# Performance work log

Measured on AMD Instinct MI355X. Metric: run time of the kernel, lower is better.

## Reference

```python
import jax, jax.numpy as jnp
import numpy as np

NEG_SLOPE = 0.2  # PyG GATConv default leaky_relu slope

def _glorot(key, shape):
    fan_in, fan_out = shape[0], shape[1]
    lim = jnp.sqrt(6.0 / (fan_in + fan_out))
    return jax.random.uniform(key, shape, jnp.float32, -lim, lim)

def setup_inputs() -> dict:
    key = jax.random.key(0)
    ks = jax.random.split(key, 16)
    N, E, S = 20000, 640000, 32
    in_dim, hid, out = 384, 128, 64
    inp = {
        'persona_x': jax.random.normal(ks[0], (N, in_dim), jnp.float32),
        'persona_edge_index': jax.random.randint(ks[1], (2, E), 0, N, jnp.int64),
        'story_x': jax.random.normal(ks[2], (S, N, in_dim), jnp.float32),
        'story_edge_index': jax.random.randint(ks[3], (S, 2, E), 0, N, jnp.int64),
    }
    # persona GAT params
    inp['p_W1'] = _glorot(ks[4], (in_dim, hid)); inp['p_a1'] = _glorot(ks[5], (2 * hid, 1)).reshape(2 * hid)
    inp['p_b1'] = jnp.zeros((hid,), jnp.float32)
    inp['p_W2'] = _glorot(ks[6], (hid, out)); inp['p_a2'] = _glorot(ks[7], (2 * out, 1)).reshape(2 * out)
    inp['p_b2'] = jnp.zeros((out,), jnp.float32)
    # story GAT params
    inp['s_W1'] = _glorot(ks[8], (in_dim, hid)); inp['s_a1'] = _glorot(ks[9], (2 * hid, 1)).reshape(2 * hid)
    inp['s_b1'] = jnp.zeros((hid,), jnp.float32)
    inp['s_W2'] = _glorot(ks[10], (hid, out)); inp['s_a2'] = _glorot(ks[11], (2 * out, 1)).reshape(2 * out)
    inp['s_b2'] = jnp.zeros((out,), jnp.float32)
    inp['temperature'] = jnp.asarray(0.07, jnp.float32)
    return inp

def gat_conv(x, edge_index, W, a, b):
    # x: [N, F_in], edge_index: [2, E] (row 0 = src, row 1 = dst), PyG GATConv heads=1
    N = x.shape[0]
    h = x @ W  # [N, F_out]
    src, dst = edge_index[0], edge_index[1]
    F_out = h.shape[1]
    # PyG adds self-loops by default
    loops = jnp.arange(N, dtype=src.dtype)
    src = jnp.concatenate([src, loops]); dst = jnp.concatenate([dst, loops])
    h_src = h[src]  # [E+N, F_out]
    h_dst = h[dst]
    # alpha = leaky_relu(a_src . h_src + a_dst . h_dst)
    a_src, a_dst = a[:F_out], a[F_out:]
    e = jax.nn.leaky_relu(h_src @ a_src + h_dst @ a_dst, NEG_SLOPE)  # [E+N]
    # segment softmax over destination nodes
    e_max = jax.ops.segment_max(e, dst, num_segments=N)
    e_exp = jnp.exp(e - e_max[dst])
    denom = jax.ops.segment_sum(e_exp, dst, num_segments=N)
    alpha = e_exp / (denom[dst] + 1e-16)
    out = jax.ops.segment_sum(h_src * alpha[:, None], dst, num_segments=N)
    return out + b

def persona_gnn(x, edge_index, W1, a1, b1, W2, a2, b2):
    h = jax.nn.relu(gat_conv(x, edge_index, W1, a1, b1))
    h = gat_conv(h, edge_index, W2, a2, b2)
    return h.mean(axis=0)  # [out_dim]

def reference(persona_x, persona_edge_index, story_x, story_edge_index,
              p_W1, p_a1, p_b1, p_W2, p_a2, p_b2,
              s_W1, s_a1, s_b1, s_W2, s_a2, s_b2, temperature):
    persona_emb = persona_gnn(persona_x, persona_edge_index, p_W1, p_a1, p_b1, p_W2, p_a2, p_b2)
    story_embs = jax.vmap(lambda x, ei: persona_gnn(x, ei, s_W1, s_a1, s_b1, s_W2, s_a2, s_b2))(
        story_x, story_edge_index)  # [S, out_dim]
    p = persona_emb / jnp.linalg.norm(persona_emb)
    s = story_embs / jnp.linalg.norm(story_embs, axis=1, keepdims=True)
    return (s @ p) / temperature  # [S]
```

## Files before the change

kernel.cpp:

```cpp
#include <hip/hip_runtime.h>
#include <cstdio>
#include <cstdint>

constexpr int N_NODES = 20000;
constexpr int E_EDGES = 640000;
constexpr int S_STORIES = 32;
constexpr int G_TOT = 33;
constexpr int IN_DIM = 384;
constexpr int HID = 128;
constexpr int F_OUT = 64;
constexpr float NEG_SLOPE = 0.2f;

constexpr int EPB = 8192;
constexpr int NB = (E_EDGES + EPB - 1) / EPB;
constexpr int NBUCK = (N_NODES + 63) / 64;

typedef short short8 __attribute__((ext_vector_type(8)));
typedef float f32x4 __attribute__((ext_vector_type(4)));

__device__ __forceinline__ float leaky(float x) { return x > 0.f ? x : NEG_SLOPE * x; }

__device__ __forceinline__ uint32_t f2bf(float x) {
    uint32_t u = __builtin_bit_cast(uint32_t, x);
    return (u + 0x7fffu + ((u >> 16) & 1u)) >> 16;
}
__device__ __forceinline__ uint32_t pk2(float lo, float hi) { return (f2bf(hi) << 16) | f2bf(lo); }
__device__ __forceinline__ float bflo(uint32_t u) { return __builtin_bit_cast(float, u << 16); }
__device__ __forceinline__ float bfhi(uint32_t u) { return __builtin_bit_cast(float, u & 0xffff0000u); }

__global__ void zero_kernel(float* __restrict__ b, size_t nb) {
    size_t i = (size_t)blockIdx.x * blockDim.x + threadIdx.x;
    if (i < nb) b[i] = 0.f;
}

__global__ __launch_bounds__(256) void csr_count(const int* __restrict__ pei, const int* __restrict__ sei,
                                                 unsigned* __restrict__ C) {
    int blk = blockIdx.x;
    int g = blk / NB, k = blk - g * NB;
    const int* ei = (g == 0) ? pei : sei + (size_t)(g - 1) * 2 * E_EDGES;
    const int* dstp = ei + E_EDGES;
    int lo = k * EPB, hi = min(lo + EPB, E_EDGES);
    __shared__ unsigned cnt[NBUCK];
    for (int i = threadIdx.x; i < NBUCK; i += 256) cnt[i] = 0;
    __syncthreads();
    for (int i = lo + threadIdx.x; i < hi; i += 256)
        atomicAdd(&cnt[dstp[i] >> 6], 1u);
    __syncthreads();
    unsigned* Cb = C + ((size_t)g * NB + k) * NBUCK;
    for (int i = threadIdx.x; i < NBUCK; i += 256) Cb[i] = cnt[i];
}

__global__ __launch_bounds__(512) void csr_scan(unsigned* __restrict__ C, unsigned* __restrict__ BB) {
    int g = blockIdx.x;
    __shared__ unsigned tot[NBUCK + 1];
    unsigned* Cg = C + (size_t)g * NB * NBUCK;
    for (int b = threadIdx.x; b < NBUCK; b += 512) {
        unsigned s = 0;
        for (int k = 0; k < NB; ++k) s += Cg[(size_t)k * NBUCK + b];
        tot[b] = s;
    }
    __syncthreads();
    if (threadIdx.x == 0) {
        unsigned run = 0;
        for (int b = 0; b < NBUCK; ++b) { unsigned t = tot[b]; tot[b] = run; run += t; }
        tot[NBUCK] = run;
    }
    __syncthreads();
    for (int b = threadIdx.x; b <= NBUCK; b += 512) BB[(size_t)g * (NBUCK + 1) + b] = tot[b];
    for (int b = threadIdx.x; b < NBUCK; b += 512) {
        unsigned run = tot[b];
        for (int k = 0; k < NB; ++k) {
            unsigned t = Cg[(size_t)k * NBUCK + b];
            Cg[(size_t)k * NBUCK + b] = run;
            run += t;
        }
    }
}

__global__ __launch_bounds__(256) void csr_bucket(const int* __restrict__ pei, const int* __restrict__ sei,
                                                  const unsigned* __restrict__ C, unsigned* __restrict__ tmp) {
    int blk = blockIdx.x;
    int g = blk / NB, k = blk - g * NB;
    const int* ei = (g == 0) ? pei : sei + (size_t)(g - 1) * 2 * E_EDGES;
    int lo = k * EPB, hi = min(lo + EPB, E_EDGES);
    __shared__ unsigned off[NBUCK];
    const unsigned* Cb = C + ((size_t)g * NB + k) * NBUCK;
    for (int i = threadIdx.x; i < NBUCK; i += 256) off[i] = Cb[i];
    __syncthreads();
    unsigned* tg = tmp + (size_t)g * E_EDGES;
    for (int i = lo + threadIdx.x; i < hi; i += 256) {
        int s = ei[i], d = ei[E_EDGES + i];
        unsigned r = atomicAdd(&off[d >> 6], 1u);
        tg[r] = ((unsigned)(d & 63) << 15) | (unsigned)s;
    }
}

__global__ __launch_bounds__(256) void csr_fine(const unsigned* __restrict__ tmp, const unsigned* __restrict__ BB,
                                                int* __restrict__ row, int* __restrict__ csr_src) {
    int blk = blockIdx.x;
    int g = blk / NBUCK, b = blk - g * NBUCK;
    unsigned lo = BB[(size_t)g * (NBUCK + 1) + b];
    unsigned hi = BB[(size_t)g * (NBUCK + 1) + b + 1];
    __shared__ unsigned cnt[64];
    __shared__ unsigned pos[64];
    if (threadIdx.x < 64) cnt[threadIdx.x] = 0;
    __syncthreads();
    const unsigned* tg = tmp + (size_t)g * E_EDGES;
    for (unsigned i = lo + threadIdx.x; i < hi; i += 256)
        atomicAdd(&cnt[(tg[i] >> 15) & 63], 1u);
    __syncthreads();
    if (threadIdx.x < 64) {
        unsigned v = cnt[threadIdx.x];
        unsigned inc = v;
#pragma unroll
        for (int o = 1; o < 64; o <<= 1) {
            unsigned u = __shfl_up(inc, o);
            if ((int)threadIdx.x >= o) inc += u;
        }
        unsigned e = inc - v;
        pos[threadIdx.x] = lo + e;
        int n = b * 64 + (int)threadIdx.x;
        if (n <= N_NODES) row[(size_t)g * (N_NODES + 1) + n] = (int)(lo + e);
    }
    __syncthreads();
    for (unsigned i = lo + threadIdx.x; i < hi; i += 256) {
        unsigned v = tg[i];
        unsigned r = atomicAdd(&pos[(v >> 15) & 63], 1u);
        csr_src[(size_t)g * E_EDGES + r] = (int)(v & 0x7fffu);
    }
}

__global__ void wprep_kernel(const float* __restrict__ pW1, const float* __restrict__ sW1,
                             const float* __restrict__ pW2, const float* __restrict__ sW2,
                             short* __restrict__ w1t, short* __restrict__ w2t) {
    constexpr int N1 = 2 * HID * IN_DIM;
    constexpr int N2 = 2 * F_OUT * HID;
    int idx = blockIdx.x * 256 + threadIdx.x;
    if (idx < N1) {
        int t = idx / (HID * IN_DIM);
        int r = idx % (HID * IN_DIM);
        int col = r / IN_DIM, k = r % IN_DIM;
        const float* W = t ? sW1 : pW1;
        float v = W[(size_t)k * HID + col];
        uint32_t hi = f2bf(v);
        float fhi = __builtin_bit_cast(float, hi << 16);
        w1t[idx]      = (short)hi;
        w1t[idx + N1] = (short)f2bf(v - fhi);
    } else if (idx < N1 + N2) {
        int j = idx - N1;
        int t = j / (F_OUT * HID);
        int r = j % (F_OUT * HID);
        int col = r / HID, k = r % HID;
        const float* W = t ? sW2 : pW2;
        float v = W[(size_t)k * F_OUT + col];
        uint32_t hi = f2bf(v);
        float fhi = __builtin_bit_cast(float, hi << 16);
        w2t[j]      = (short)hi;
        w2t[j + N2] = (short)f2bf(v - fhi);
    }
}

template<int KDIM, int NCOL, bool CVT>
__global__ __launch_bounds__(256) void mm_mfma(const void* __restrict__ pXv, const void* __restrict__ sXv,
                                               const short* __restrict__ wt,
                                               const float* __restrict__ pa, const float* __restrict__ sa,
                                               uint16_t* __restrict__ outb,
                                               float* __restrict__ as_, float* __restrict__ ad_) {
    constexpr int BPG = (N_NODES + 127) / 128;
    constexpr int NT = NCOL / 16;
    int g = blockIdx.x / BPG;
    int brow = (blockIdx.x % BPG) * 128;
    const short* wtg = wt + (g ? (size_t)NCOL * KDIM : 0);
    __shared__ __align__(16) short As[128 * 40];
    __shared__ __align__(16) short Bh[NCOL * 40];
    __shared__ __align__(16) short Bl[NCOL * 40];
    int tid = threadIdx.x;
    int w = tid >> 6, l = tid & 63;
    int lr = l & 15, kq = l >> 4;
    f32x4 acc[2][NT] = {};
    for (int k0 = 0; k0 < KDIM; k0 += 32) {
        if (CVT) {
            const float* X = (g == 0) ? (const float*)pXv
                                      : (const float*)sXv + (size_t)(g - 1) * N_NODES * KDIM;
#pragma unroll
            for (int i = 0; i < 4; ++i) {
                int v = tid + i * 256;
                int r = v >> 3, q = v & 7;
                float4 xv = make_float4(0.f, 0.f, 0.f, 0.f);
                if (brow + r < N_NODES)
                    xv = *(const float4*)(X + (size_t)(brow + r) * KDIM + k0 + q * 4);
                uint2 pkd; pkd.x = pk2(xv.x, xv.y); pkd.y = pk2(xv.z, xv.w);
                *(uint2*)(As + r * 40 + q * 4) = pkd;
            }
        } else {
            const uint16_t* X = (g == 0) ? (const uint16_t*)pXv
                                         : (const uint16_t*)sXv + (size_t)(g - 1) * N_NODES * KDIM;
#pragma unroll
            for (int i = 0; i < 2; ++i) {
                int v = tid + i * 256;
                int r = v >> 2, q = v & 3;
                uint4 xv = make_uint4(0u, 0u, 0u, 0u);
                if (brow + r < N_NODES)
                    xv = *(const uint4*)(X + (size_t)(brow + r) * KDIM + k0 + q * 8);
                *(uint4*)(As + r * 40 + q * 8) = xv;
            }
        }
        for (int v = tid; v < NCOL * 4; v += 256) {
            int r = v >> 2, q = v & 3;
            const short* srcp = wtg + (size_t)r * KDIM + k0 + q * 8;
            *(uint4*)(Bh + r * 40 + q * 8) = *(const uint4*)srcp;
            *(uint4*)(Bl + r * 40 + q * 8) = *(const uint4*)(srcp + (size_t)2 * NCOL * KDIM);
        }
        __syncthreads();
        short8 a0 = *(const short8*)(As + (w * 32 + lr) * 40 + kq * 8);
        short8 a1 = *(const short8*)(As + (w * 32 + 16 + lr) * 40 + kq * 8);
#pragma unroll
        for (int ct = 0; ct < NT; ++ct) {
            short8 bh = *(const short8*)(Bh + (ct * 16 + lr) * 40 + kq * 8);
            short8 bl = *(const short8*)(Bl + (ct * 16 + lr) * 40 + kq * 8);
            acc[0][ct] = __builtin_amdgcn_mfma_f32_16x16x32_bf16(a0, bh, acc[0][ct], 0, 0, 0);
            acc[0][ct] = __builtin_amdgcn_mfma_f32_16x16x32_bf16(a0, bl, acc[0][ct], 0, 0, 0);
            acc[1][ct] = __builtin_amdgcn_mfma_f32_16x16x32_bf16(a1, bh, acc[1][ct], 0, 0, 0);
            acc[1][ct] = __builtin_amdgcn_mfma_f32_16x16x32_bf16(a1, bl, acc[1][ct], 0, 0, 0);
        }
        __syncthreads();
    }
    const float* av = (g == 0) ? pa : sa;
    float aS[NT], aD[NT];
#pragma unroll
    for (int ct = 0; ct < NT; ++ct) {
        aS[ct] = av[ct * 16 + lr];
        aD[ct] = av[NCOL + ct * 16 + lr];
    }
#pragma unroll
    for (int rt = 0; rt < 2; ++rt) {
#pragma unroll
        for (int i = 0; i < 4; ++i) {
            int node = brow + w * 32 + rt * 16 + kq * 4 + i;
            float s = 0.f, d = 0.f;
#pragma unroll
            for (int ct = 0; ct < NT; ++ct) {
                float h = acc[rt][ct][i];
                s += h * aS[ct];
                d += h * aD[ct];
                if (node < N_NODES)
                    outb[((size_t)g * N_NODES + node) * NCOL + ct * 16 + lr] = (uint16_t)f2bf(h);
            }
#pragma unroll
            for (int off = 1; off < 16; off <<= 1) { s += __shfl_xor(s, off); d += __shfl_xor(d, off); }
            if (lr == 0 && node < N_NODES) {
                as_[(size_t)g * N_NODES + node] = s;
                ad_[(size_t)g * N_NODES + node] = d;
            }
        }
    }
}

__global__ __launch_bounds__(256) void agg128_kernel(const uint32_t* __restrict__ hb,
                                                     const float* __restrict__ as_, const float* __restrict__ ad_,
                                                     const int* __restrict__ row, const int* __restrict__ csr_src,
                                                     const float* __restrict__ pb, const float* __restrict__ sb,
                                                     uint32_t* __restrict__ h1p) {
    int node = blockIdx.x * 4 + (threadIdx.x >> 6);
    int g = node / N_NODES;
    int n = node - g * N_NODES;
    int lane = threadIdx.x & 63;
    int start = row[(size_t)g * (N_NODES + 1) + n];
    int end   = row[(size_t)g * (N_NODES + 1) + n + 1];
    const int* src = csr_src + (size_t)g * E_EDGES;
    const float* asg = as_ + (size_t)g * N_NODES;
    const uint32_t* hg = hb + (size_t)g * N_NODES * 64;
    float ad_d = ad_[node];
    float e_self = leaky(asg[n] + ad_d);
    int grp = lane >> 4;
    int f = lane & 15;
    const uint32_t* hf = hg + f * 4;
    float m = e_self, denomp = 0.f;
    float a0 = 0.f, a1 = 0.f, a2 = 0.f, a3 = 0.f, a4 = 0.f, a5 = 0.f, a6 = 0.f, a7 = 0.f;
    for (int j0 = start; j0 < end; j0 += 64) {
        int j = j0 + lane;
        float e = -3.0e38f; int s0 = 0;
        if (j < end) { s0 = src[j]; e = leaky(asg[s0] + ad_d); }
        float cmax = e;
#pragma unroll
        for (int off = 32; off; off >>= 1) cmax = fmaxf(cmax, __shfl_xor(cmax, off));
        if (cmax > m) {
            float sc = __expf(m - cmax);
            denomp *= sc;
            a0 *= sc; a1 *= sc; a2 *= sc; a3 *= sc; a4 *= sc; a5 *= sc; a6 *= sc; a7 *= sc;
            m = cmax;
        }
        float w0 = (j < end) ? __expf(e - m) : 0.f;
        denomp += w0;
        int cnt = min(64, end - j0);
        for (int t = 0; t < cnt; t += 8) {
            float w_[2]; int s_[2];
#pragma unroll
            for (int u = 0; u < 2; ++u) {
                int tt = t + u * 4 + grp;
                w_[u] = __shfl(w0, tt);
                s_[u] = __shfl(s0, tt);
            }
            uint4 hv_[2];
#pragma unroll
            for (int u = 0; u < 2; ++u)
                hv_[u] = *(const uint4*)(hf + (size_t)s_[u] * 64);
#pragma unroll
            for (int u = 0; u < 2; ++u) {
                float w = w_[u]; uint4 hv = hv_[u];
                a0 += w * bflo(hv.x); a1 += w * bfhi(hv.x);
                a2 += w * bflo(hv.y); a3 += w * bfhi(hv.y);
                a4 += w * bflo(hv.z); a5 += w * bfhi(hv.z);
                a6 += w * bflo(hv.w); a7 += w * bfhi(hv.w);
            }
        }
    }
#pragma unroll
    for (int off = 32; off; off >>= 1) denomp += __shfl_xor(denomp, off);
#pragma unroll
    for (int off = 16; off <= 32; off <<= 1) {
        a0 += __shfl_xor(a0, off); a1 += __shfl_xor(a1, off);
        a2 += __shfl_xor(a2, off); a3 += __shfl_xor(a3, off);
        a4 += __shfl_xor(a4, off); a5 += __shfl_xor(a5, off);
        a6 += __shfl_xor(a6, off); a7 += __shfl_xor(a7, off);
    }
    if (lane < 16) {
        float wself = __expf(e_self - m);
        float inv = 1.f / (denomp + wself + 1e-16f);
        uint4 hv = *(const uint4*)(hg + (size_t)n * 64 + lane * 4);
        const float* b = (g == 0) ? pb : sb;
        float4 b0 = *(const float4*)(b + lane * 8);
        float4 b1 = *(const float4*)(b + lane * 8 + 4);
        float o0 = fmaxf((a0 + wself * bflo(hv.x)) * inv + b0.x, 0.f);
        float o1 = fmaxf((a1 + wself * bfhi(hv.x)) * inv + b0.y, 0.f);
        float o2 = fmaxf((a2 + wself * bflo(hv.y)) * inv + b0.z, 0.f);
        float o3 = fmaxf((a3 + wself * bfhi(hv.y)) * inv + b0.w, 0.f);
        float o4 = fmaxf((a4 + wself * bflo(hv.z)) * inv + b1.x, 0.f);
        float o5 = fmaxf((a5 + wself * bfhi(hv.z)) * inv + b1.y, 0.f);
        float o6 = fmaxf((a6 + wself * bflo(hv.w)) * inv + b1.z, 0.f);
        float o7 = fmaxf((a7 + wself * bfhi(hv.w)) * inv + b1.w, 0.f);
        uint4 o; o.x = pk2(o0, o1); o.y = pk2(o2, o3); o.z = pk2(o4, o5); o.w = pk2(o6, o7);
        *(uint4*)(h1p + (size_t)node * 64 + lane * 4) = o;
    }
}

__global__ __launch_bounds__(256) void agg64_kernel(const uint32_t* __restrict__ hb,
                                                    const float* __restrict__ as_, const float* __restrict__ ad_,
                                                    const int* __restrict__ row, const int* __restrict__ csr_src,
                                                    const float* __restrict__ pb, const float* __restrict__ sb,
                                                    float* __restrict__ outp) {
    int node = blockIdx.x * 4 + (threadIdx.x >> 6);
    int g = node / N_NODES;
    int n = node - g * N_NODES;
    int lane = threadIdx.x & 63;
    int start = row[(size_t)g * (N_NODES + 1) + n];
    int end   = row[(size_t)g * (N_NODES + 1) + n + 1];
    const int* src = csr_src + (size_t)g * E_EDGES;
    const float* asg = as_ + (size_t)g * N_NODES;
    const uint32_t* hg = hb + (size_t)g * N_NODES * 32;
    float ad_d = ad_[node];
    float e_self = leaky(asg[n] + ad_d);
    int grp = lane >> 4;
    int f = lane & 15;
    const uint32_t* hf = hg + f * 2;
    float m = e_self, denomp = 0.f;
    float a0 = 0.f, a1 = 0.f, a2 = 0.f, a3 = 0.f;
    for (int j0 = start; j0 < end; j0 += 64) {
        int j = j0 + lane;
        float e = -3.0e38f; int s0 = 0;
        if (j < end) { s0 = src[j]; e = leaky(asg[s0] + ad_d); }
        float cmax = e;
#pragma unroll
        for (int off = 32; off; off >>= 1) cmax = fmaxf(cmax, __shfl_xor(cmax, off));
        if (cmax > m) {
            float sc = __expf(m - cmax);
            denomp *= sc;
            a0 *= sc; a1 *= sc; a2 *= sc; a3 *= sc;
            m = cmax;
        }
        float w0 = (j < end) ? __expf(e - m) : 0.f;
        denomp += w0;
        int cnt = min(64, end - j0);
        for (int t = 0; t < cnt; t += 16) {
            float w_[4]; int s_[4];
#pragma unroll
            for (int u = 0; u < 4; ++u) {
                int tt = t + u * 4 + grp;
                w_[u] = __shfl(w0, tt);
                s_[u] = __shfl(s0, tt);
            }
            uint2 hv_[4];
#pragma unroll
            for (int u = 0; u < 4; ++u)
                hv_[u] = *(const uint2*)(hf + (size_t)s_[u] * 32);
#pragma unroll
            for (int u = 0; u < 4; ++u) {
                float w = w_[u]; uint2 hv = hv_[u];
                a0 += w * bflo(hv.x); a1 += w * bfhi(hv.x);
                a2 += w * bflo(hv.y); a3 += w * bfhi(hv.y);
            }
        }
    }
#pragma unroll
    for (int off = 32; off; off >>= 1) denomp += __shfl_xor(denomp, off);
#pragma unroll
    for (int off = 16; off <= 32; off <<= 1) {
        a0 += __shfl_xor(a0, off); a1 += __shfl_xor(a1, off);
        a2 += __shfl_xor(a2, off); a3 += __shfl_xor(a3, off);
    }
    if (lane < 16) {
        float wself = __expf(e_self - m);
        float inv = 1.f / (denomp + wself + 1e-16f);
        uint2 hv = *(const uint2*)(hg + (size_t)n * 32 + lane * 2);
        const float* b = (g == 0) ? pb : sb;
        float4 bv = *(const float4*)(b + lane * 4);
        float4 o;
        o.x = (a0 + wself * bflo(hv.x)) * inv + bv.x;
        o.y = (a1 + wself * bfhi(hv.x)) * inv + bv.y;
        o.z = (a2 + wself * bflo(hv.y)) * inv + bv.z;
        o.w = (a3 + wself * bfhi(hv.y)) * inv + bv.w;
        *(float4*)(outp + (size_t)node * 64 + lane * 4) = o;
    }
}

__global__ __launch_bounds__(256) void mean_kernel(const float* __restrict__ out2, float* __restrict__ emb) {
    constexpr int CH = 32;
    int g = blockIdx.x / CH, chunk = blockIdx.x % CH;
    int f = threadIdx.x & 63, sub = threadIdx.x >> 6;
    float acc = 0.f;
    for (int n = chunk * 4 + sub; n < N_NODES; n += CH * 4)
        acc += out2[((size_t)g * N_NODES + n) * 64 + f];
    __shared__ float red[256];
    red[threadIdx.x] = acc;
    __syncthreads();
    if (sub == 0) {
        float s = red[f] + red[64 + f] + red[128 + f] + red[192 + f];
        atomicAdd(&emb[g * 64 + f], s * (1.f / N_NODES));
    }
}

__global__ __launch_bounds__(64) void final_kernel(const float* __restrict__ emb,
                                                   const float* __restrict__ temp, float* __restrict__ out) {
    int lane = threadIdx.x;
    float pe = emb[lane];
    float pp = pe * pe;
#pragma unroll
    for (int off = 32; off; off >>= 1) pp += __shfl_xor(pp, off);
    float t = temp[0];
    float pn = sqrtf(pp);
    for (int s_i = 0; s_i < S_STORIES; ++s_i) {
        float se = emb[(1 + s_i) * 64 + lane];
        float ss = se * se;
        float dt = se * pe;
#pragma unroll
        for (int off = 32; off; off >>= 1) { ss += __shfl_xor(ss, off); dt += __shfl_xor(dt, off); }
        if (lane == 0) out[s_i] = dt / (sqrtf(ss) * pn * t);
    }
}

extern "C" void kernel_launch(void* const* d_in, const int* in_sizes, int n_in,
                              void* d_out, int out_size, void* d_ws, size_t ws_size,
                              hipStream_t stream) {
    const float* persona_x = (const float*)d_in[0];
    const int*   pei       = (const int*)d_in[1];
    const float* story_x   = (const float*)d_in[2];
    const int*   sei       = (const int*)d_in[3];
    const float* p_W1 = (const float*)d_in[4];
    const float* p_a1 = (const float*)d_in[5];
    const float* p_b1 = (const float*)d_in[6];
    const float* p_W2 = (const float*)d_in[7];
    const float* p_a2 = (const float*)d_in[8];
    const float* p_b2 = (const float*)d_in[9];
    const float* s_W1 = (const float*)d_in[10];
    const float* s_a1 = (const float*)d_in[11];
    const float* s_b1 = (const float*)d_in[12];
    const float* s_W2 = (const float*)d_in[13];
    const float* s_a2 = (const float*)d_in[14];
    const float* s_b2 = (const float*)d_in[15];
    const float* temp = (const float*)d_in[16];
    float* out = (float*)d_out;

    char* ws = (char*)d_ws;
    size_t off = 0;
    auto alloc = [&](size_t bytes) { char* p = ws + off; off += (bytes + 255) & ~(size_t)255; return p; };
    uint32_t* hb1  = (uint32_t*)alloc((size_t)G_TOT * N_NODES * 64 * 4);
    uint32_t* h1p  = (uint32_t*)alloc((size_t)G_TOT * N_NODES * 64 * 4);
    uint32_t* hb2  = (uint32_t*)alloc((size_t)G_TOT * N_NODES * 32 * 4);
    float* as_     = (float*)alloc((size_t)G_TOT * N_NODES * 4);
    float* ad_     = (float*)alloc((size_t)G_TOT * N_NODES * 4);
    int*   csr_row = (int*)  alloc((size_t)G_TOT * (N_NODES + 1) * 4);
    int*   csr_src = (int*)  alloc((size_t)G_TOT * E_EDGES * 4);
    float* emb     = (float*)alloc((size_t)G_TOT * 64 * 4);
    short* w1t     = (short*)alloc((size_t)2 * 2 * HID * IN_DIM * 2);
    short* w2t     = (short*)alloc((size_t)2 * 2 * F_OUT * HID * 2);
    if (off > ws_size) {
        fprintf(stderr, "kernel_launch: ws too small: need %zu have %zu\n", off, ws_size);
        return;
    }
    unsigned* tmp = (unsigned*)hb1;
    unsigned* C   = (unsigned*)h1p;
    unsigned* BB  = (unsigned*)h1p + (size_t)G_TOT * NB * NBUCK;
    float* out2   = (float*)hb1;

    constexpr int BPG = (N_NODES + 127) / 128;
    const int NODE_BLOCKS = G_TOT * N_NODES / 4;

    zero_kernel<<<(G_TOT * 64 + 255) / 256, 256, 0, stream>>>(emb, (size_t)G_TOT * 64);
    wprep_kernel<<<(2 * HID * IN_DIM + 2 * F_OUT * HID + 255) / 256, 256, 0, stream>>>(p_W1, s_W1, p_W2, s_W2, w1t, w2t);
    csr_count <<<G_TOT * NB, 256, 0, stream>>>(pei, sei, C);
    csr_scan  <<<G_TOT, 512, 0, stream>>>(C, BB);
    csr_bucket<<<G_TOT * NB, 256, 0, stream>>>(pei, sei, C, tmp);
    csr_fine  <<<G_TOT * NBUCK, 256, 0, stream>>>(tmp, BB, csr_row, csr_src);

    mm_mfma<IN_DIM, HID, true><<<G_TOT * BPG, 256, 0, stream>>>(persona_x, story_x, w1t, p_a1, s_a1,
                                                                (uint16_t*)hb1, as_, ad_);
    agg128_kernel<<<NODE_BLOCKS, 256, 0, stream>>>(hb1, as_, ad_, csr_row, csr_src, p_b1, s_b1, h1p);

    const uint16_t* h1p16 = (const uint16_t*)h1p;
    mm_mfma<HID, F_OUT, false><<<G_TOT * BPG, 256, 0, stream>>>(h1p16, h1p16 + (size_t)N_NODES * HID, w2t, p_a2, s_a2,
                                                                (uint16_t*)hb2, as_, ad_);
    agg64_kernel<<<NODE_BLOCKS, 256, 0, stream>>>(hb2, as_, ad_, csr_row, csr_src, p_b2, s_b2, out2);

    mean_kernel<<<G_TOT * 32, 256, 0, stream>>>(out2, emb);
    final_kernel<<<1, 64, 0, stream>>>(emb, temp, out);
}
```

Measured before the change: 2.161 ms.

## Fuse CSR build stages with first-layer GEMM into shared heterogeneous launches

Merges zeroing, weight prep and edge counting into one launch. It then splits the first-layer MFMA GEMM into two halves that run in the same grids as the CSR bucket and fine-sort phases, so the memory-bound sort work overlaps with the compute-bound GEMM. The tmp buffer moves to hb2 so it no longer conflicts with the GEMM output in hb1. This cuts the number of launches and idle tail time, at the cost of larger shared-memory footprints for the CSR blocks, which may lower their occupancy.

```diff
diff --git a/kernel.cpp b/kernel.cpp
--- a/kernel.cpp
+++ b/kernel.cpp
@@ -15,6 +15,16 @@
 constexpr int NB = (E_EDGES + EPB - 1) / EPB;
 constexpr int NBUCK = (N_NODES + 63) / 64;
 
+constexpr int CNT_BLOCKS  = G_TOT * NB;
+constexpr int WPREP_ELEMS = 2 * HID * IN_DIM + 2 * F_OUT * HID;
+constexpr int WPREP_BLOCKS = (WPREP_ELEMS + 255) / 256;
+constexpr int ZERO_BLOCKS = (G_TOT * 64 + 255) / 256;
+constexpr int MM_BPG = (N_NODES + 127) / 128;
+constexpr int MM_BLOCKS = G_TOT * MM_BPG;
+constexpr int MM_HALF_A = MM_BLOCKS / 2;
+constexpr int MM_HALF_B = MM_BLOCKS - MM_HALF_A;
+constexpr int FINE_BLOCKS = G_TOT * NBUCK;
+
 typedef short short8 __attribute__((ext_vector_type(8)));
 typedef float f32x4 __attribute__((ext_vector_type(4)));
 
@@ -28,19 +38,14 @@
 __device__ __forceinline__ float bflo(uint32_t u) { return __builtin_bit_cast(float, u << 16); }
 __device__ __forceinline__ float bfhi(uint32_t u) { return __builtin_bit_cast(float, u & 0xffff0000u); }
 
-__global__ void zero_kernel(float* __restrict__ b, size_t nb) {
-    size_t i = (size_t)blockIdx.x * blockDim.x + threadIdx.x;
-    if (i < nb) b[i] = 0.f;
-}
-
-__global__ __launch_bounds__(256) void csr_count(const int* __restrict__ pei, const int* __restrict__ sei,
-                                                 unsigned* __restrict__ C) {
-    int blk = blockIdx.x;
+
+__device__ __forceinline__ void count_body(int blk, unsigned* cnt,
+                                           const int* __restrict__ pei, const int* __restrict__ sei,
+                                           unsigned* __restrict__ C) {
     int g = blk / NB, k = blk - g * NB;
     const int* ei = (g == 0) ? pei : sei + (size_t)(g - 1) * 2 * E_EDGES;
     const int* dstp = ei + E_EDGES;
     int lo = k * EPB, hi = min(lo + EPB, E_EDGES);
-    __shared__ unsigned cnt[NBUCK];
     for (int i = threadIdx.x; i < NBUCK; i += 256) cnt[i] = 0;
     __syncthreads();
     for (int i = lo + threadIdx.x; i < hi; i += 256)
@@ -50,92 +55,13 @@
     for (int i = threadIdx.x; i < NBUCK; i += 256) Cb[i] = cnt[i];
 }
 
-__global__ __launch_bounds__(512) void csr_scan(unsigned* __restrict__ C, unsigned* __restrict__ BB) {
-    int g = blockIdx.x;
-    __shared__ unsigned tot[NBUCK + 1];
-    unsigned* Cg = C + (size_t)g * NB * NBUCK;
-    for (int b = threadIdx.x; b < NBUCK; b += 512) {
-        unsigned s = 0;
-        for (int k = 0; k < NB; ++k) s += Cg[(size_t)k * NBUCK + b];
-        tot[b] = s;
-    }
-    __syncthreads();
-    if (threadIdx.x == 0) {
-        unsigned run = 0;
-        for (int b = 0; b < NBUCK; ++b) { unsigned t = tot[b]; tot[b] = run; run += t; }
-        tot[NBUCK] = run;
-    }
-    __syncthreads();
-    for (int b = threadIdx.x; b <= NBUCK; b += 512) BB[(size_t)g * (NBUCK + 1) + b] = tot[b];
-    for (int b = threadIdx.x; b < NBUCK; b += 512) {
-        unsigned run = tot[b];
-        for (int k = 0; k < NB; ++k) {
-            unsigned t = Cg[(size_t)k * NBUCK + b];
-            Cg[(size_t)k * NBUCK + b] = run;
-            run += t;
-        }
-    }
-}
-
-__global__ __launch_bounds__(256) void csr_bucket(const int* __restrict__ pei, const int* __restrict__ sei,
-                                                  const unsigned* __restrict__ C, unsigned* __restrict__ tmp) {
-    int blk = blockIdx.x;
-    int g = blk / NB, k = blk - g * NB;
-    const int* ei = (g == 0) ? pei : sei + (size_t)(g - 1) * 2 * E_EDGES;
-    int lo = k * EPB, hi = min(lo + EPB, E_EDGES);
-    __shared__ unsigned off[NBUCK];
-    const unsigned* Cb = C + ((size_t)g * NB + k) * NBUCK;
-    for (int i = threadIdx.x; i < NBUCK; i += 256) off[i] = Cb[i];
-    __syncthreads();
-    unsigned* tg = tmp + (size_t)g * E_EDGES;
-    for (int i = lo + threadIdx.x; i < hi; i += 256) {
-        int s = ei[i], d = ei[E_EDGES + i];
-        unsigned r = atomicAdd(&off[d >> 6], 1u);
-        tg[r] = ((unsigned)(d & 63) << 15) | (unsigned)s;
-    }
-}
-
-__global__ __launch_bounds__(256) void csr_fine(const unsigned* __restrict__ tmp, const unsigned* __restrict__ BB,
-                                                int* __restrict__ row, int* __restrict__ csr_src) {
-    int blk = blockIdx.x;
-    int g = blk / NBUCK, b = blk - g * NBUCK;
-    unsigned lo = BB[(size_t)g * (NBUCK + 1) + b];
-    unsigned hi = BB[(size_t)g * (NBUCK + 1) + b + 1];
-    __shared__ unsigned cnt[64];
-    __shared__ unsigned pos[64];
-    if (threadIdx.x < 64) cnt[threadIdx.x] = 0;
-    __syncthreads();
-    const unsigned* tg = tmp + (size_t)g * E_EDGES;
-    for (unsigned i = lo + threadIdx.x; i < hi; i += 256)
-        atomicAdd(&cnt[(tg[i] >> 15) & 63], 1u);
-    __syncthreads();
-    if (threadIdx.x < 64) {
-        unsigned v = cnt[threadIdx.x];
-        unsigned inc = v;
-#pragma unroll
-        for (int o = 1; o < 64; o <<= 1) {
-            unsigned u = __shfl_up(inc, o);
-            if ((int)threadIdx.x >= o) inc += u;
-        }
-        unsigned e = inc - v;
-        pos[threadIdx.x] = lo + e;
-        int n = b * 64 + (int)threadIdx.x;
-        if (n <= N_NODES) row[(size_t)g * (N_NODES + 1) + n] = (int)(lo + e);
-    }
-    __syncthreads();
-    for (unsigned i = lo + threadIdx.x; i < hi; i += 256) {
-        unsigned v = tg[i];
-        unsigned r = atomicAdd(&pos[(v >> 15) & 63], 1u);
-        csr_src[(size_t)g * E_EDGES + r] = (int)(v & 0x7fffu);
-    }
-}
-
-__global__ void wprep_kernel(const float* __restrict__ pW1, const float* __restrict__ sW1,
-                             const float* __restrict__ pW2, const float* __restrict__ sW2,
-                             short* __restrict__ w1t, short* __restrict__ w2t) {
+__device__ __forceinline__ void wprep_body(int blk,
+                                           const float* __restrict__ pW1, const float* __restrict__ sW1,
+                                           const float* __restrict__ pW2, const float* __restrict__ sW2,
+                                           short* __restrict__ w1t, short* __restrict__ w2t) {
     constexpr int N1 = 2 * HID * IN_DIM;
     constexpr int N2 = 2 * F_OUT * HID;
-    int idx = blockIdx.x * 256 + threadIdx.x;
+    int idx = blk * 256 + threadIdx.x;
     if (idx < N1) {
         int t = idx / (HID * IN_DIM);
         int r = idx % (HID * IN_DIM);
@@ -160,20 +86,70 @@
     }
 }
 
+__device__ __forceinline__ void bucket_body(int blk, unsigned* off,
+                                            const int* __restrict__ pei, const int* __restrict__ sei,
+                                            const unsigned* __restrict__ C, unsigned* __restrict__ tmp) {
+    int g = blk / NB, k = blk - g * NB;
+    const int* ei = (g == 0) ? pei : sei + (size_t)(g - 1) * 2 * E_EDGES;
+    int lo = k * EPB, hi = min(lo + EPB, E_EDGES);
+    const unsigned* Cb = C + ((size_t)g * NB + k) * NBUCK;
+    for (int i = threadIdx.x; i < NBUCK; i += 256) off[i] = Cb[i];
+    __syncthreads();
+    unsigned* tg = tmp + (size_t)g * E_EDGES;
+    for (int i = lo + threadIdx.x; i < hi; i += 256) {
+        int s = ei[i], d = ei[E_EDGES + i];
+        unsigned r = atomicAdd(&off[d >> 6], 1u);
+        tg[r] = ((unsigned)(d & 63) << 15) | (unsigned)s;
+    }
+}
+
+__device__ __forceinline__ void fine_body(int blk, unsigned* cnt, unsigned* pos,
+                                          const unsigned* __restrict__ tmp, const unsigned* __restrict__ BB,
+                                          int* __restrict__ row, int* __restrict__ csr_src) {
+    int g = blk / NBUCK, b = blk - g * NBUCK;
+    unsigned lo = BB[(size_t)g * (NBUCK + 1) + b];
+    unsigned hi = BB[(size_t)g * (NBUCK + 1) + b + 1];
+    if (threadIdx.x < 64) cnt[threadIdx.x] = 0;
+    __syncthreads();
+    const unsigned* tg = tmp + (size_t)g * E_EDGES;
+    for (unsigned i = lo + threadIdx.x; i < hi; i += 256)
+        atomicAdd(&cnt[(tg[i] >> 15) & 63], 1u);
+    __syncthreads();
+    if (threadIdx.x < 64) {
+        unsigned v = cnt[threadIdx.x];
+        unsigned inc = v;
+#pragma unroll
+        for (int o = 1; o < 64; o <<= 1) {
+            unsigned u = __shfl_up(inc, o);
+            if ((int)threadIdx.x >= o) inc += u;
+        }
+        unsigned e = inc - v;
+        pos[threadIdx.x] = lo + e;
+        int n = b * 64 + (int)threadIdx.x;
+        if (n <= N_NODES) row[(size_t)g * (N_NODES + 1) + n] = (int)(lo + e);
+    }
+    __syncthreads();
+    for (unsigned i = lo + threadIdx.x; i < hi; i += 256) {
+        unsigned v = tg[i];
+        unsigned r = atomicAdd(&pos[(v >> 15) & 63], 1u);
+        csr_src[(size_t)g * E_EDGES + r] = (int)(v & 0x7fffu);
+    }
+}
+
 template<int KDIM, int NCOL, bool CVT>
-__global__ __launch_bounds__(256) void mm_mfma(const void* __restrict__ pXv, const void* __restrict__ sXv,
-                                               const short* __restrict__ wt,
-                                               const float* __restrict__ pa, const float* __restrict__ sa,
-                                               uint16_t* __restrict__ outb,
-                                               float* __restrict__ as_, float* __restrict__ ad_) {
-    constexpr int BPG = (N_NODES + 127) / 128;
+__device__ __forceinline__ void mm_body(int bid, char* smemc,
+                                        const void* __restrict__ pXv, const void* __restrict__ sXv,
+                                        const short* __restrict__ wt,
+                                        const float* __restrict__ pa, const float* __restrict__ sa,
+                                        uint16_t* __restrict__ outb,
+                                        float* __restrict__ as_, float* __restrict__ ad_) {
     constexpr int NT = NCOL / 16;
-    int g = blockIdx.x / BPG;
-    int brow = (blockIdx.x % BPG) * 128;
+    int g = bid / MM_BPG;
+    int brow = (bid % MM_BPG) * 128;
     const short* wtg = wt + (g ? (size_t)NCOL * KDIM : 0);
-    __shared__ __align__(16) short As[128 * 40];
-    __shared__ __align__(16) short Bh[NCOL * 40];
-    __shared__ __align__(16) short Bl[NCOL * 40];
+    short* As = (short*)smemc;
+    short* Bh = As + 128 * 40;
+    short* Bl = Bh + NCOL * 40;
     int tid = threadIdx.x;
     int w = tid >> 6, l = tid & 63;
     int lr = l & 15, kq = l >> 4;
@@ -254,6 +230,96 @@
             }
         }
     }
+}
+
+
+__global__ __launch_bounds__(256) void k0_kernel(const int* __restrict__ pei, const int* __restrict__ sei,
+                                                 unsigned* __restrict__ C,
+                                                 const float* __restrict__ pW1, const float* __restrict__ sW1,
+                                                 const float* __restrict__ pW2, const float* __restrict__ sW2,
+                                                 short* __restrict__ w1t, short* __restrict__ w2t,
+                                                 float* __restrict__ emb) {
+    __shared__ unsigned cnt[NBUCK];
+    int bid = blockIdx.x;
+    if (bid < CNT_BLOCKS) {
+        count_body(bid, cnt, pei, sei, C);
+    } else if (bid < CNT_BLOCKS + WPREP_BLOCKS) {
+        wprep_body(bid - CNT_BLOCKS, pW1, sW1, pW2, sW2, w1t, w2t);
+    } else {
+        int idx = (bid - CNT_BLOCKS - WPREP_BLOCKS) * 256 + threadIdx.x;
+        if (idx < G_TOT * 64) emb[idx] = 0.f;
+    }
+}
+
+__global__ __launch_bounds__(512) void csr_scan(unsigned* __restrict__ C, unsigned* __restrict__ BB) {
+    int g = blockIdx.x;
+    __shared__ unsigned tot[NBUCK + 1];
+    unsigned* Cg = C + (size_t)g * NB * NBUCK;
+    for (int b = threadIdx.x; b < NBUCK; b += 512) {
+        unsigned s = 0;
+        for (int k = 0; k < NB; ++k) s += Cg[(size_t)k * NBUCK + b];
+        tot[b] = s;
+    }
+    __syncthreads();
+    if (threadIdx.x == 0) {
+        unsigned run = 0;
+        for (int b = 0; b < NBUCK; ++b) { unsigned t = tot[b]; tot[b] = run; run += t; }
+        tot[NBUCK] = run;
+    }
+    __syncthreads();
+    for (int b = threadIdx.x; b <= NBUCK; b += 512) BB[(size_t)g * (NBUCK + 1) + b] = tot[b];
+    for (int b = threadIdx.x; b < NBUCK; b += 512) {
+        unsigned run = tot[b];
+        for (int k = 0; k < NB; ++k) {
+            unsigned t = Cg[(size_t)k * NBUCK + b];
+            Cg[(size_t)k * NBUCK + b] = run;
+            run += t;
+        }
+    }
+}
+
+__global__ __launch_bounds__(256) void mm_bucket_kernel(const void* __restrict__ pXv, const void* __restrict__ sXv,
+                                                        const short* __restrict__ wt,
+                                                        const float* __restrict__ pa, const float* __restrict__ sa,
+                                                        uint16_t* __restrict__ outb,
+                                                        float* __restrict__ as_, float* __restrict__ ad_,
+                                                        const int* __restrict__ pei, const int* __restrict__ sei,
+                                                        const unsigned* __restrict__ C, unsigned* __restrict__ tmp) {
+    constexpr int SM = (128 * 40 + HID * 40 * 2) * 2;
+    __shared__ __align__(16) char smem[SM];
+    int bid = blockIdx.x;
+    if (bid < MM_HALF_A)
+        mm_body<IN_DIM, HID, true>(bid, smem, pXv, sXv, wt, pa, sa, outb, as_, ad_);
+    else
+        bucket_body(bid - MM_HALF_A, (unsigned*)smem, pei, sei, C, tmp);
+}
+
+__global__ __launch_bounds__(256) void mm_fine_kernel(const void* __restrict__ pXv, const void* __restrict__ sXv,
+                                                      const short* __restrict__ wt,
+                                                      const float* __restrict__ pa, const float* __restrict__ sa,
+                                                      uint16_t* __restrict__ outb,
+                                                      float* __restrict__ as_, float* __restrict__ ad_,
+                                                      const unsigned* __restrict__ tmp, const unsigned* __restrict__ BB,
+                                                      int* __restrict__ row, int* __restrict__ csr_src) {
+    constexpr int SM = (128 * 40 + HID * 40 * 2) * 2;
+    __shared__ __align__(16) char smem[SM];
+    int bid = blockIdx.x;
+    if (bid < MM_HALF_B)
+        mm_body<IN_DIM, HID, true>(bid + MM_HALF_A, smem, pXv, sXv, wt, pa, sa, outb, as_, ad_);
+    else {
+        unsigned* cnt = (unsigned*)smem;
+        fine_body(bid - MM_HALF_B, cnt, cnt + 64, tmp, BB, row, csr_src);
+    }
+}
+
+__global__ __launch_bounds__(256) void mm_only_kernel(const void* __restrict__ pXv, const void* __restrict__ sXv,
+                                                      const short* __restrict__ wt,
+                                                      const float* __restrict__ pa, const float* __restrict__ sa,
+                                                      uint16_t* __restrict__ outb,
+                                                      float* __restrict__ as_, float* __restrict__ ad_) {
+    constexpr int SM = (128 * 40 + F_OUT * 40 * 2) * 2;
+    __shared__ __align__(16) char smem[SM];
+    mm_body<HID, F_OUT, false>(blockIdx.x, smem, pXv, sXv, wt, pa, sa, outb, as_, ad_);
 }
 
 __global__ __launch_bounds__(256) void agg128_kernel(const uint32_t* __restrict__ hb,
@@ -497,28 +563,26 @@
         fprintf(stderr, "kernel_launch: ws too small: need %zu have %zu\n", off, ws_size);
         return;
     }
-    unsigned* tmp = (unsigned*)hb1;
+    unsigned* tmp = (unsigned*)hb2;
     unsigned* C   = (unsigned*)h1p;
     unsigned* BB  = (unsigned*)h1p + (size_t)G_TOT * NB * NBUCK;
     float* out2   = (float*)hb1;
 
-    constexpr int BPG = (N_NODES + 127) / 128;
     const int NODE_BLOCKS = G_TOT * N_NODES / 4;
 
-    zero_kernel<<<(G_TOT * 64 + 255) / 256, 256, 0, stream>>>(emb, (size_t)G_TOT * 64);
-    wprep_kernel<<<(2 * HID * IN_DIM + 2 * F_OUT * HID + 255) / 256, 256, 0, stream>>>(p_W1, s_W1, p_W2, s_W2, w1t, w2t);
-    csr_count <<<G_TOT * NB, 256, 0, stream>>>(pei, sei, C);
-    csr_scan  <<<G_TOT, 512, 0, stream>>>(C, BB);
-    csr_bucket<<<G_TOT * NB, 256, 0, stream>>>(pei, sei, C, tmp);
-    csr_fine  <<<G_TOT * NBUCK, 256, 0, stream>>>(tmp, BB, csr_row, csr_src);
-
-    mm_mfma<IN_DIM, HID, true><<<G_TOT * BPG, 256, 0, stream>>>(persona_x, story_x, w1t, p_a1, s_a1,
-                                                                (uint16_t*)hb1, as_, ad_);
+    k0_kernel<<<CNT_BLOCKS + WPREP_BLOCKS + ZERO_BLOCKS, 256, 0, stream>>>(
+        pei, sei, C, p_W1, s_W1, p_W2, s_W2, w1t, w2t, emb);
+    csr_scan<<<G_TOT, 512, 0, stream>>>(C, BB);
+    mm_bucket_kernel<<<MM_HALF_A + CNT_BLOCKS, 256, 0, stream>>>(
+        persona_x, story_x, w1t, p_a1, s_a1, (uint16_t*)hb1, as_, ad_, pei, sei, C, tmp);
+    mm_fine_kernel<<<MM_HALF_B + FINE_BLOCKS, 256, 0, stream>>>(
+        persona_x, story_x, w1t, p_a1, s_a1, (uint16_t*)hb1, as_, ad_, tmp, BB, csr_row, csr_src);
+
     agg128_kernel<<<NODE_BLOCKS, 256, 0, stream>>>(hb1, as_, ad_, csr_row, csr_src, p_b1, s_b1, h1p);
 
     const uint16_t* h1p16 = (const uint16_t*)h1p;
-    mm_mfma<HID, F_OUT, false><<<G_TOT * BPG, 256, 0, stream>>>(h1p16, h1p16 + (size_t)N_NODES * HID, w2t, p_a2, s_a2,
-                                                                (uint16_t*)hb2, as_, ad_);
+    mm_only_kernel<<<MM_BLOCKS, 256, 0, stream>>>(h1p16, h1p16 + (size_t)N_NODES * HID, w2t, p_a2, s_a2,
+                                                  (uint16_t*)hb2, as_, ad_);
     agg64_kernel<<<NODE_BLOCKS, 256, 0, stream>>>(hb2, as_, ad_, csr_row, csr_src, p_b2, s_b2, out2);
 
     mean_kernel<<<G_TOT * 32, 256, 0, stream>>>(out2, emb);
```

Result: faster. 1.967 ms (-8.9%).
